# Performance work log

Hardware: AMD Instinct MI355X
Metric: run time of the kernel (lower is better)

Reference implementation:

```python
import jax, jax.numpy as jnp
import numpy as np
from math import ceil, sqrt

# Inner module: Linear(2048,4096)+ReLU, Linear(4096,4096)+ReLU, Linear(4096,2048)
D_IN, D_H, D_OUT = 2048, 4096, 2048
BATCH = 4096
# named_modules() order: each Linear yields weight then bias; ReLU skipped
SHAPES = [(D_H, D_IN), (D_H,), (D_H, D_H), (D_H,), (D_OUT, D_H), (D_OUT,)]
NUM_P = sum(int(np.prod(s)) for s in SHAPES)  # 33_566_720
SIZE_N = ceil(sqrt(NUM_P))                    # 5794
SIZE_M = ceil(1.0 * SIZE_N / 2)               # 2897 (compress = 1.0)


def setup_inputs() -> dict:
    key = jax.random.key(0)
    k1, k2, k3 = jax.random.split(key, 3)
    k = sqrt(12) / 2 * SIZE_M ** (-0.25)  # norm_V init bound
    V1 = jax.random.uniform(k1, (SIZE_N, SIZE_M), jnp.float32, -k, k)
    V2 = jax.random.uniform(k2, (SIZE_M, SIZE_N), jnp.float32, -k, k)
    x = jax.random.normal(k3, (BATCH, D_IN), jnp.float32)
    return {"x": x, "V1": V1, "V2": V2}


def _unpack(Vf):
    # scatter-copy: contiguous slices of flattened V -> weights/biases in traversal order
    params, i = [], 0
    for s in SHAPES:
        n = int(np.prod(s))
        params.append(Vf[i:i + n].reshape(s))
        i += n
    return params


def reference(x, V1, V2):
    # WandBtoV: low-rank reconstruction then per-element copy into weights (fused here)
    Vf = (V1 @ V2).reshape(-1)  # [SIZE_N*SIZE_N]; only first NUM_P elements used
    W1, b1, W2, b2, W3, b3 = _unpack(Vf)
    h = jax.nn.relu(x @ W1.T + b1)   # [B, D_H]
    h = jax.nn.relu(h @ W2.T + b2)   # [B, D_H]
    return h @ W3.T + b3             # [B, D_OUT]
```

## Files before the change

kernel.cpp:

```cpp
#include <hip/hip_runtime.h>
#include <stdint.h>

typedef __attribute__((ext_vector_type(8)))  __bf16 bf16x8;
typedef __attribute__((ext_vector_type(16))) float  f32x16;
typedef unsigned short u16;
typedef __attribute__((ext_vector_type(8))) unsigned short u16x8;

#define GLOBAL_AS __attribute__((address_space(1)))
#define LDS_AS    __attribute__((address_space(3)))

__device__ __forceinline__ void load_lds16(const void* g, void* l) {
    __builtin_amdgcn_global_load_lds((const GLOBAL_AS void*)g, (LDS_AS void*)l, 16, 0, 0);
}

__device__ __forceinline__ u16 f2bf(float f) {
    union { float f; uint32_t u; } v; v.f = f;
    uint32_t r = v.u + 0x7FFFu + ((v.u >> 16) & 1u);
    return (u16)(r >> 16);
}
__device__ __forceinline__ float b2f(u16 b) {
    union { uint32_t u; float f; } v; v.u = ((uint32_t)b) << 16;
    return v.f;
}

__global__ void k_conv_pad(const float* __restrict__ in, u16* __restrict__ out,
                           int rIn, int cIn, int cOut, int total8) {
    int idx = blockIdx.x * blockDim.x + threadIdx.x;
    if (idx >= total8) return;
    int c8n = cOut >> 3;
    int r  = idx / c8n;
    int c0 = (idx - r * c8n) << 3;
    u16x8 o;
#pragma unroll
    for (int j = 0; j < 8; ++j) {
        int c = c0 + j;
        o[j] = (r < rIn && c < cIn) ? f2bf(in[(size_t)r * cIn + c]) : (u16)0;
    }
    *(u16x8*)(out + (size_t)r * cOut + c0) = o;
}

__global__ void k_transpose_conv(const float* __restrict__ in, u16* __restrict__ out,
                                 int kIn, int nIn, int kOut) {
    __shared__ float tile[32][33];
    int k0 = blockIdx.x * 32, n0 = blockIdx.y * 32;
    int tx = threadIdx.x, ty = threadIdx.y;
#pragma unroll
    for (int i = 0; i < 4; ++i) {
        int k = k0 + ty + i * 8, n = n0 + tx;
        tile[ty + i * 8][tx] = (k < kIn && n < nIn) ? in[(size_t)k * nIn + n] : 0.f;
    }
    __syncthreads();
#pragma unroll
    for (int i = 0; i < 4; ++i) {
        int n = n0 + ty + i * 8, k = k0 + tx;
        out[(size_t)n * kOut + k] = f2bf(tile[tx][ty + i * 8]);
    }
}

template <int MODE>
__global__ __launch_bounds__(256, 4) void k_gemm_bt(
    const u16* __restrict__ A, const u16* __restrict__ B,
    const u16* __restrict__ bias, void* __restrict__ Cv,
    int K, int ldc, int mReal, int nReal) {
    (void)bias;
    __shared__ __align__(16) char lds[32768];
    char* As = lds;
    char* Bs = lds + 16384;

    const int tid  = threadIdx.x;
    const int w    = tid >> 6, lane = tid & 63;
    const int l31  = lane & 31, hi = lane >> 5;
    const int wm   = (w & 1) * 64, wn = (w >> 1) * 64;
    const int bm   = blockIdx.y * 128, bn = blockIdx.x * 128;

    const int srcRow = tid >> 3;
    const int srcCol = (tid & 7) ^ (srcRow & 7);
    const u16* aSrc = A + (size_t)(bm + srcRow) * K + (srcCol << 3);
    const u16* bSrc = B + (size_t)(bn + srcRow) * K + (srcCol << 3);
    char* aDst = As + ((tid & ~63) << 4);
    char* bDst = Bs + ((tid & ~63) << 4);

    const int aRow0 = (wm + l31) * 128;
    const int aRow1 = (wm + 32 + l31) * 128;
    const int bRow0 = (wn + l31) * 128;
    const int bRow1 = (wn + 32 + l31) * 128;

    f32x16 acc[2][2];
#pragma unroll
    for (int i = 0; i < 2; ++i)
#pragma unroll
        for (int j = 0; j < 2; ++j) acc[i][j] = (f32x16)(0.f);

    for (int k0 = 0; k0 < K; k0 += 64) {
#pragma unroll
        for (int t = 0; t < 4; ++t) {
            load_lds16(aSrc + (size_t)(t * 32) * K, aDst + t * 4096);
            load_lds16(bSrc + (size_t)(t * 32) * K, bDst + t * 4096);
        }
        aSrc += 64; bSrc += 64;
        __syncthreads();
#pragma unroll
        for (int ks = 0; ks < 4; ++ks) {
            const int swz = (((ks * 2 + hi) ^ (l31 & 7)) << 4);
            bf16x8 af[2], bfr[2];
            af[0]  = *(const bf16x8*)(As + aRow0 + swz);
            af[1]  = *(const bf16x8*)(As + aRow1 + swz);
            bfr[0] = *(const bf16x8*)(Bs + bRow0 + swz);
            bfr[1] = *(const bf16x8*)(Bs + bRow1 + swz);
#pragma unroll
            for (int mi = 0; mi < 2; ++mi)
#pragma unroll
                for (int ni = 0; ni < 2; ++ni)
                    acc[mi][ni] = __builtin_amdgcn_mfma_f32_32x32x16_bf16(
                        af[mi], bfr[ni], acc[mi][ni], 0, 0, 0);
        }
        __syncthreads();
    }

    float bv[2];
    if (MODE >= 1) {
#pragma unroll
        for (int ni = 0; ni < 2; ++ni) bv[ni] = b2f(bias[bn + wn + ni * 32 + l31]);
    }
#pragma unroll
    for (int mi = 0; mi < 2; ++mi) {
#pragma unroll
        for (int reg = 0; reg < 16; ++reg) {
            int row = bm + wm + mi * 32 + (reg & 3) + 8 * (reg >> 2) + 4 * hi;
#pragma unroll
            for (int ni = 0; ni < 2; ++ni) {
                int col = bn + wn + ni * 32 + l31;
                float v = acc[mi][ni][reg];
                if (MODE == 0) {
                    if (row < mReal && col < nReal)
                        ((u16*)Cv)[(size_t)row * ldc + col] = f2bf(v);
                } else if (MODE == 1) {
                    v += bv[ni];
                    v = v > 0.f ? v : 0.f;
                    ((u16*)Cv)[(size_t)row * ldc + col] = f2bf(v);
                } else {
                    ((float*)Cv)[(size_t)row * ldc + col] = v + bv[ni];
                }
            }
        }
    }
}


#define BARRIER() do { asm volatile("" ::: "memory"); \
                       __builtin_amdgcn_s_barrier(); \
                       asm volatile("" ::: "memory"); } while (0)
#define LGKM0()   do { asm volatile("s_waitcnt lgkmcnt(0)" ::: "memory"); \
                       __builtin_amdgcn_sched_barrier(0); } while (0)
#define VMCNT(n)  asm volatile("s_waitcnt vmcnt(" #n ")" ::: "memory")

#define STAGE8(bb, ko) do { \
    _Pragma("unroll") for (int t = 0; t < 4; ++t) \
        load_lds16(aS + (ko) + (size_t)(t * 64) * K, (bb) + wOff + t * 8192); \
    _Pragma("unroll") for (int t = 0; t < 4; ++t) \
        load_lds16(bS + (ko) + (size_t)(t * 64) * K, (bb) + 32768 + wOff + t * 8192); \
} while (0)

#define PH_RD_A(bb, mh) do { \
    _Pragma("unroll") for (int m2 = 0; m2 < 2; ++m2) \
    _Pragma("unroll") for (int ks = 0; ks < 4; ++ks) \
        fa[m2][ks] = *(const bf16x8*)((bb) + aRowB + ((mh) * 2 + m2) * 4096 + (chB ^ (ks << 5))); \
} while (0)

#define PH_RD_B(bb, n) do { \
    _Pragma("unroll") for (int ks = 0; ks < 4; ++ks) \
        fb[n][ks] = *(const bf16x8*)((bb) + bRowB + (n) * 4096 + (chB ^ (ks << 5))); \
} while (0)

#define PH_MM(mh, n) do { \
    __builtin_amdgcn_s_setprio(1); \
    _Pragma("unroll") for (int m2 = 0; m2 < 2; ++m2) \
    _Pragma("unroll") for (int ks = 0; ks < 4; ++ks) \
        acc[(mh) * 2 + m2][n] = __builtin_amdgcn_mfma_f32_32x32x16_bf16( \
            fa[m2][ks], fb[n][ks], acc[(mh) * 2 + m2][n], 0, 0, 0); \
    __builtin_amdgcn_s_setprio(0); \
} while (0)

template <int MODE>
__global__ __launch_bounds__(512, 2) void k_gemm256(
    const u16* __restrict__ A, const u16* __restrict__ B,
    const u16* __restrict__ bias, void* __restrict__ Cv,
    int K, int ldc, int mReal, int nReal, int gx) {
    __shared__ __align__(16) char lds[131072];

    const int tid  = threadIdx.x;
    const int w    = tid >> 6, lane = tid & 63;
    const int l31  = lane & 31, hi = lane >> 5;
    const int wr   = w & 1, wc = w >> 1;

    const int nwg = (int)gridDim.x;
    const int q   = nwg >> 3, r = nwg & 7;
    const int xcd = (int)blockIdx.x & 7, lid = (int)blockIdx.x >> 3;
    const int wg  = (xcd < r ? xcd * (q + 1) : r * (q + 1) + (xcd - r) * q) + lid;
    const int bm  = (wg / gx) * 256;
    const int bn  = (wg % gx) * 256;

    char* const buf0 = lds;
    char* const buf1 = lds + 65536;

    const int srcRow = tid >> 3;
    const int srcCh  = (tid & 7) ^ (srcRow & 7);
    const u16* const aS = A + (size_t)(bm + srcRow) * K + (srcCh << 3);
    const u16* const bS = B + (size_t)(bn + srcRow) * K + (srcCh << 3);
    const int wOff = (tid & ~63) << 4;

    const int aRowB = (wr * 128 + l31) * 128;
    const int bRowB = 32768 + (wc * 64 + l31) * 128;
    const int chB   = (hi ^ (l31 & 7)) << 4;

    f32x16 acc[4][2];
#pragma unroll
    for (int i = 0; i < 4; ++i)
#pragma unroll
        for (int j = 0; j < 2; ++j) acc[i][j] = (f32x16)(0.f);

    bf16x8 fa[2][4], fb[2][4];

    STAGE8(buf0, 0);
    STAGE8(buf1, 64);
    VMCNT(8);
    BARRIER();

    const int nIt = K >> 7;
    size_t ko = 128;
#pragma unroll 1
    for (int it = 0; it < nIt; ++it) {
        const bool notLast = (it != nIt - 1);
        PH_RD_A(buf0, 0); PH_RD_B(buf0, 0);
        BARRIER(); LGKM0(); PH_MM(0, 0); BARRIER();
        PH_RD_B(buf0, 1);
        BARRIER(); LGKM0(); PH_MM(0, 1); BARRIER();
        PH_RD_A(buf0, 1);
        BARRIER(); LGKM0(); PH_MM(1, 1); BARRIER();
        if (notLast) { STAGE8(buf0, ko); }
        BARRIER(); PH_MM(1, 0);
        if (notLast) { VMCNT(8); } else { VMCNT(0); }
        BARRIER();
        PH_RD_A(buf1, 0); PH_RD_B(buf1, 0);
        BARRIER(); LGKM0(); PH_MM(0, 0); BARRIER();
        PH_RD_B(buf1, 1);
        BARRIER(); LGKM0(); PH_MM(0, 1); BARRIER();
        PH_RD_A(buf1, 1);
        BARRIER(); LGKM0(); PH_MM(1, 1); BARRIER();
        if (notLast) { STAGE8(buf1, ko + 64); ko += 128; }
        BARRIER(); PH_MM(1, 0);
        if (notLast) { VMCNT(8); }
        BARRIER();
    }

    float bv[2];
    if (MODE >= 1) {
#pragma unroll
        for (int ni = 0; ni < 2; ++ni) bv[ni] = b2f(bias[bn + wc * 64 + ni * 32 + l31]);
    }
#pragma unroll
    for (int mi = 0; mi < 4; ++mi) {
#pragma unroll
        for (int reg = 0; reg < 16; ++reg) {
            const int row = bm + wr * 128 + mi * 32 + (reg & 3) + 8 * (reg >> 2) + 4 * hi;
#pragma unroll
            for (int ni = 0; ni < 2; ++ni) {
                const int col = bn + wc * 64 + ni * 32 + l31;
                float v = acc[mi][ni][reg];
                if (MODE == 0) {
                    if (row < mReal && col < nReal)
                        ((u16*)Cv)[(size_t)row * ldc + col] = f2bf(v);
                } else if (MODE == 1) {
                    v += bv[ni];
                    v = v > 0.f ? v : 0.f;
                    ((u16*)Cv)[(size_t)row * ldc + col] = f2bf(v);
                } else {
                    ((float*)Cv)[(size_t)row * ldc + col] = v + bv[ni];
                }
            }
        }
    }
}

extern "C" void kernel_launch(void* const* d_in, const int* in_sizes, int n_in,
                              void* d_out, int out_size, void* d_ws, size_t ws_size,
                              hipStream_t stream) {
    (void)in_sizes; (void)n_in; (void)out_size; (void)ws_size;
    const float* x  = (const float*)d_in[0];
    const float* V1 = (const float*)d_in[1];
    const float* V2 = (const float*)d_in[2];

    char* ws = (char*)d_ws;
    u16* Vf   = (u16*)(ws);
    u16* V1b  = (u16*)(ws + 67141120);
    u16* V2bT = (u16*)(ws + 67141120 + 34668544);
    u16* Xb   = (u16*)(ws + 67141120 + 2 * 34668544);
    u16* H1   = V1b;
    u16* H2   = V2bT;

    k_conv_pad<<<8464, 256, 0, stream>>>(V1, V1b, 5794, 2897, 2944, 5888 * 2944 / 8);
    k_transpose_conv<<<dim3(92, 184), dim3(32, 8), 0, stream>>>(V2, V2bT, 2897, 5794, 2944);
    k_conv_pad<<<4096, 256, 0, stream>>>(x, Xb, 4096, 2048, 2048, 4096 * 2048 / 8);

    k_gemm256<0><<<529, 512, 0, stream>>>(V1b, V2bT, nullptr, Vf,
                                          2944, 5794, 5794, 5794, 23);
    k_gemm256<1><<<256, 512, 0, stream>>>(Xb, Vf + 0, Vf + 8388608, H1,
                                          2048, 4096, 4096, 4096, 16);
    k_gemm256<1><<<256, 512, 0, stream>>>(H1, Vf + 8392704, Vf + 25169920, H2,
                                          4096, 4096, 4096, 4096, 16);
    k_gemm_bt<2><<<dim3(16, 32), 256, 0, stream>>>(H2, Vf + 25174016, Vf + 33562624, d_out,
                                                   4096, 2048, 4096, 2048);
}
```

Before: 790.5 us.

## Restructure GEMM main loop into per-k-slice phases and add persistent tile loop

```diff
diff --git a/kernel.cpp b/kernel.cpp
--- a/kernel.cpp
+++ b/kernel.cpp
@@ -152,40 +152,46 @@
                        asm volatile("" ::: "memory"); } while (0)
 #define LGKM0()   do { asm volatile("s_waitcnt lgkmcnt(0)" ::: "memory"); \
                        __builtin_amdgcn_sched_barrier(0); } while (0)
-#define VMCNT(n)  asm volatile("s_waitcnt vmcnt(" #n ")" ::: "memory")
-
-#define STAGE8(bb, ko) do { \
+#define VMCNT0()  do { asm volatile("s_waitcnt vmcnt(0)" ::: "memory"); \
+                       __builtin_amdgcn_sched_barrier(0); } while (0)
+
+#define STAGE8(bb, koff) do { \
     _Pragma("unroll") for (int t = 0; t < 4; ++t) \
-        load_lds16(aS + (ko) + (size_t)(t * 64) * K, (bb) + wOff + t * 8192); \
+        load_lds16(aS + (koff) + (size_t)(t * 64) * K, (bb) + wOff + t * 8192); \
     _Pragma("unroll") for (int t = 0; t < 4; ++t) \
-        load_lds16(bS + (ko) + (size_t)(t * 64) * K, (bb) + 32768 + wOff + t * 8192); \
+        load_lds16(bS + (koff) + (size_t)(t * 64) * K, (bb) + 32768 + wOff + t * 8192); \
 } while (0)
 
-#define PH_RD_A(bb, mh) do { \
-    _Pragma("unroll") for (int m2 = 0; m2 < 2; ++m2) \
-    _Pragma("unroll") for (int ks = 0; ks < 4; ++ks) \
-        fa[m2][ks] = *(const bf16x8*)((bb) + aRowB + ((mh) * 2 + m2) * 4096 + (chB ^ (ks << 5))); \
-} while (0)
-
-#define PH_RD_B(bb, n) do { \
-    _Pragma("unroll") for (int ks = 0; ks < 4; ++ks) \
-        fb[n][ks] = *(const bf16x8*)((bb) + bRowB + (n) * 4096 + (chB ^ (ks << 5))); \
-} while (0)
-
-#define PH_MM(mh, n) do { \
+#define PH(bb, p, MID) do { \
+    const int co_ = chB ^ ((p) << 5); \
+    bf16x8 fa0_ = *(const bf16x8*)((bb) + aRowB +     0 + co_); \
+    bf16x8 fa1_ = *(const bf16x8*)((bb) + aRowB +  4096 + co_); \
+    bf16x8 fa2_ = *(const bf16x8*)((bb) + aRowB +  8192 + co_); \
+    bf16x8 fa3_ = *(const bf16x8*)((bb) + aRowB + 12288 + co_); \
+    bf16x8 fb0_ = *(const bf16x8*)((bb) + bRowB +     0 + co_); \
+    bf16x8 fb1_ = *(const bf16x8*)((bb) + bRowB +  4096 + co_); \
+    MID \
+    LGKM0(); \
     __builtin_amdgcn_s_setprio(1); \
-    _Pragma("unroll") for (int m2 = 0; m2 < 2; ++m2) \
-    _Pragma("unroll") for (int ks = 0; ks < 4; ++ks) \
-        acc[(mh) * 2 + m2][n] = __builtin_amdgcn_mfma_f32_32x32x16_bf16( \
-            fa[m2][ks], fb[n][ks], acc[(mh) * 2 + m2][n], 0, 0, 0); \
+    acc[0][0] = __builtin_amdgcn_mfma_f32_32x32x16_bf16(fa0_, fb0_, acc[0][0], 0, 0, 0); \
+    acc[1][0] = __builtin_amdgcn_mfma_f32_32x32x16_bf16(fa1_, fb0_, acc[1][0], 0, 0, 0); \
+    acc[2][0] = __builtin_amdgcn_mfma_f32_32x32x16_bf16(fa2_, fb0_, acc[2][0], 0, 0, 0); \
+    acc[3][0] = __builtin_amdgcn_mfma_f32_32x32x16_bf16(fa3_, fb0_, acc[3][0], 0, 0, 0); \
+    acc[0][1] = __builtin_amdgcn_mfma_f32_32x32x16_bf16(fa0_, fb1_, acc[0][1], 0, 0, 0); \
+    acc[1][1] = __builtin_amdgcn_mfma_f32_32x32x16_bf16(fa1_, fb1_, acc[1][1], 0, 0, 0); \
+    acc[2][1] = __builtin_amdgcn_mfma_f32_32x32x16_bf16(fa2_, fb1_, acc[2][1], 0, 0, 0); \
+    acc[3][1] = __builtin_amdgcn_mfma_f32_32x32x16_bf16(fa3_, fb1_, acc[3][1], 0, 0, 0); \
     __builtin_amdgcn_s_setprio(0); \
 } while (0)
+
+#define PH_PLAIN ;
+#define PH_SYNC  LGKM0(); VMCNT0(); BARRIER();
 
 template <int MODE>
 __global__ __launch_bounds__(512, 2) void k_gemm256(
     const u16* __restrict__ A, const u16* __restrict__ B,
     const u16* __restrict__ bias, void* __restrict__ Cv,
-    int K, int ldc, int mReal, int nReal, int gx) {
+    int K, int ldc, int mReal, int nReal, int gx, int nTiles) {
     __shared__ __align__(16) char lds[131072];
 
     const int tid  = threadIdx.x;
@@ -193,89 +199,77 @@
     const int l31  = lane & 31, hi = lane >> 5;
     const int wr   = w & 1, wc = w >> 1;
 
-    const int nwg = (int)gridDim.x;
-    const int q   = nwg >> 3, r = nwg & 7;
-    const int xcd = (int)blockIdx.x & 7, lid = (int)blockIdx.x >> 3;
-    const int wg  = (xcd < r ? xcd * (q + 1) : r * (q + 1) + (xcd - r) * q) + lid;
-    const int bm  = (wg / gx) * 256;
-    const int bn  = (wg % gx) * 256;
+    const int cpx = (int)gridDim.x >> 3;
+    const int wg0 = ((int)blockIdx.x & 7) * cpx + ((int)blockIdx.x >> 3);
 
     char* const buf0 = lds;
     char* const buf1 = lds + 65536;
 
     const int srcRow = tid >> 3;
     const int srcCh  = (tid & 7) ^ (srcRow & 7);
-    const u16* const aS = A + (size_t)(bm + srcRow) * K + (srcCh << 3);
-    const u16* const bS = B + (size_t)(bn + srcRow) * K + (srcCh << 3);
-    const int wOff = (tid & ~63) << 4;
+    const int wOff   = (tid & ~63) << 4;
 
     const int aRowB = (wr * 128 + l31) * 128;
     const int bRowB = 32768 + (wc * 64 + l31) * 128;
     const int chB   = (hi ^ (l31 & 7)) << 4;
 
-    f32x16 acc[4][2];
-#pragma unroll
-    for (int i = 0; i < 4; ++i)
-#pragma unroll
-        for (int j = 0; j < 2; ++j) acc[i][j] = (f32x16)(0.f);
-
-    bf16x8 fa[2][4], fb[2][4];
-
-    STAGE8(buf0, 0);
-    STAGE8(buf1, 64);
-    VMCNT(8);
-    BARRIER();
-
     const int nIt = K >> 7;
-    size_t ko = 128;
+
+    for (int v = wg0; v < nTiles; v += (int)gridDim.x) {
+        const int bm = (v / gx) * 256;
+        const int bn = (v % gx) * 256;
+        const u16* const aS = A + (size_t)(bm + srcRow) * K + (srcCh << 3);
+        const u16* const bS = B + (size_t)(bn + srcRow) * K + (srcCh << 3);
+
+        f32x16 acc[4][2];
+#pragma unroll
+        for (int i = 0; i < 4; ++i)
+#pragma unroll
+            for (int j = 0; j < 2; ++j) acc[i][j] = (f32x16)(0.f);
+
+        STAGE8(buf0, 0);
+        VMCNT0();
+        BARRIER();
+
+        size_t ko = 0;
 #pragma unroll 1
-    for (int it = 0; it < nIt; ++it) {
-        const bool notLast = (it != nIt - 1);
-        PH_RD_A(buf0, 0); PH_RD_B(buf0, 0);
-        BARRIER(); LGKM0(); PH_MM(0, 0); BARRIER();
-        PH_RD_B(buf0, 1);
-        BARRIER(); LGKM0(); PH_MM(0, 1); BARRIER();
-        PH_RD_A(buf0, 1);
-        BARRIER(); LGKM0(); PH_MM(1, 1); BARRIER();
-        if (notLast) { STAGE8(buf0, ko); }
-        BARRIER(); PH_MM(1, 0);
-        if (notLast) { VMCNT(8); } else { VMCNT(0); }
-        BARRIER();
-        PH_RD_A(buf1, 0); PH_RD_B(buf1, 0);
-        BARRIER(); LGKM0(); PH_MM(0, 0); BARRIER();
-        PH_RD_B(buf1, 1);
-        BARRIER(); LGKM0(); PH_MM(0, 1); BARRIER();
-        PH_RD_A(buf1, 1);
-        BARRIER(); LGKM0(); PH_MM(1, 1); BARRIER();
-        if (notLast) { STAGE8(buf1, ko + 64); ko += 128; }
-        BARRIER(); PH_MM(1, 0);
-        if (notLast) { VMCNT(8); }
-        BARRIER();
-    }
-
-    float bv[2];
-    if (MODE >= 1) {
-#pragma unroll
-        for (int ni = 0; ni < 2; ++ni) bv[ni] = b2f(bias[bn + wc * 64 + ni * 32 + l31]);
-    }
-#pragma unroll
-    for (int mi = 0; mi < 4; ++mi) {
-#pragma unroll
-        for (int reg = 0; reg < 16; ++reg) {
-            const int row = bm + wr * 128 + mi * 32 + (reg & 3) + 8 * (reg >> 2) + 4 * hi;
-#pragma unroll
-            for (int ni = 0; ni < 2; ++ni) {
-                const int col = bn + wc * 64 + ni * 32 + l31;
-                float v = acc[mi][ni][reg];
-                if (MODE == 0) {
-                    if (row < mReal && col < nReal)
-                        ((u16*)Cv)[(size_t)row * ldc + col] = f2bf(v);
-                } else if (MODE == 1) {
-                    v += bv[ni];
-                    v = v > 0.f ? v : 0.f;
-                    ((u16*)Cv)[(size_t)row * ldc + col] = f2bf(v);
-                } else {
-                    ((float*)Cv)[(size_t)row * ldc + col] = v + bv[ni];
+        for (int it = 0; it < nIt; ++it) {
+            STAGE8(buf1, ko + 64);
+            PH(buf0, 0, PH_PLAIN);
+            PH(buf0, 1, PH_PLAIN);
+            PH(buf0, 2, PH_PLAIN);
+            PH(buf0, 3, PH_SYNC if (it + 1 < nIt) { STAGE8(buf0, ko + 128); });
+            PH(buf1, 0, PH_PLAIN);
+            PH(buf1, 1, PH_PLAIN);
+            PH(buf1, 2, PH_PLAIN);
+            PH(buf1, 3, PH_SYNC);
+            ko += 128;
+        }
+
+        float bv[2];
+        if (MODE >= 1) {
+#pragma unroll
+            for (int ni = 0; ni < 2; ++ni) bv[ni] = b2f(bias[bn + wc * 64 + ni * 32 + l31]);
+        }
+#pragma unroll
+        for (int mi = 0; mi < 4; ++mi) {
+#pragma unroll
+            for (int reg = 0; reg < 16; ++reg) {
+                const int row = bm + wr * 128 + mi * 32 + (reg & 3) + 8 * (reg >> 2) + 4 * hi;
+#pragma unroll
+                for (int ni = 0; ni < 2; ++ni) {
+                    const int col = bn + wc * 64 + ni * 32 + l31;
+                    float vv = acc[mi][ni][reg];
+                    if (MODE == 0) {
+                        if (row < mReal && col < nReal)
+                            ((u16*)Cv)[(size_t)row * ldc + col] = f2bf(vv);
+                    } else if (MODE == 1) {
+                        vv += bv[ni];
+                        vv = vv > 0.f ? vv : 0.f;
+                        ((u16*)Cv)[(size_t)row * ldc + col] = f2bf(vv);
+                    } else {
+                        ((float*)Cv)[(size_t)row * ldc + col] = vv + bv[ni];
+                    }
                 }
             }
         }
@@ -302,12 +296,12 @@
     k_transpose_conv<<<dim3(92, 184), dim3(32, 8), 0, stream>>>(V2, V2bT, 2897, 5794, 2944);
     k_conv_pad<<<4096, 256, 0, stream>>>(x, Xb, 4096, 2048, 2048, 4096 * 2048 / 8);
 
-    k_gemm256<0><<<529, 512, 0, stream>>>(V1b, V2bT, nullptr, Vf,
-                                          2944, 5794, 5794, 5794, 23);
+    k_gemm256<0><<<512, 512, 0, stream>>>(V1b, V2bT, nullptr, Vf,
+                                          2944, 5794, 5794, 5794, 23, 529);
     k_gemm256<1><<<256, 512, 0, stream>>>(Xb, Vf + 0, Vf + 8388608, H1,
-                                          2048, 4096, 4096, 4096, 16);
+                                          2048, 4096, 4096, 4096, 16, 256);
     k_gemm256<1><<<256, 512, 0, stream>>>(H1, Vf + 8392704, Vf + 25169920, H2,
-                                          4096, 4096, 4096, 4096, 16);
+                                          4096, 4096, 4096, 4096, 16, 256);
     k_gemm_bt<2><<<dim3(16, 32), 256, 0, stream>>>(H2, Vf + 25174016, Vf + 33562624, d_out,
                                                    4096, 2048, 4096, 2048);
 }
```

After: 764.7 us. -3.3%, faster.
